# Performance work log

Hardware: AMD Instinct MI355X
Metric: run time of the kernel (lower is better)

The kernel has to match this reference:

```python
import jax, jax.numpy as jnp
import numpy as np

B, P = 4096, 32
NUM_ENTITY = 100000
NUM_METAPATH = 3
EMBED = 128
MAX_LEN = 3
C1, C2 = 128, 32


def setup_inputs() -> dict:
    key = jax.random.key(0)
    ks = jax.random.split(key, 20)
    inp = {}
    for g, L in enumerate([1, 2, 3]):
        inp[f"ent{L}"] = jax.random.randint(ks[3 * g], (B, P, L + 1), 0, NUM_ENTITY, dtype=jnp.int32)
        inp[f"mid{L}"] = jax.random.randint(ks[3 * g + 1], (B, P, L), 0, NUM_METAPATH, dtype=jnp.int32)
        inp[f"counts{L}"] = jax.random.uniform(ks[3 * g + 2], (B, P), jnp.float32, 0.5, 1.5)
    # parameters
    inp["E"] = jax.random.normal(ks[9], (NUM_ENTITY, EMBED), jnp.float32) * 0.02
    inp["W"] = jax.random.normal(ks[10], (NUM_METAPATH, EMBED), jnp.float32) * 0.1 + 1.0
    inp["Bm"] = jax.random.normal(ks[11], (NUM_METAPATH, EMBED), jnp.float32) * 0.02
    d_in = 2 * EMBED * MAX_LEN  # 768
    inp["W1"] = jax.random.normal(ks[12], (d_in, C1), jnp.float32) * (1.0 / np.sqrt(d_in))
    inp["b1"] = jnp.zeros((C1,), jnp.float32)
    inp["W2"] = jax.random.normal(ks[13], (C1, C2), jnp.float32) * (1.0 / np.sqrt(C1))
    inp["b2"] = jnp.zeros((C2,), jnp.float32)
    inp["W3"] = jax.random.normal(ks[14], (C2, 1), jnp.float32) * (1.0 / np.sqrt(C2))
    inp["b3"] = jnp.zeros((1,), jnp.float32)
    return inp


def _group_output(E, W, Bm, ents, mids, counts):
    """Vectorized forward_path over [B, P] paths of fixed length L, then
    count-weighted average over the P paths. ents: [B,P,L+1], mids: [B,P,L]."""
    L = mids.shape[-1]
    # forward direction
    x = E[ents[..., 0]]  # [B,P,EMBED]
    y = x
    for i in range(L):
        y = E[ents[..., i + 1]]
        x = jax.nn.relu(x * W[mids[..., i]] * y + Bm[mids[..., i]])
    out1 = x
    # backward direction: original code reuses stale y (embed of last entity)
    x = E[ents[..., L]]
    for i in reversed(range(L)):
        x = jax.nn.relu(x * W[mids[..., i]] * y + Bm[mids[..., i]])
    out2 = x
    path_out = jnp.concatenate([out1, out2], axis=-1)  # [B,P,2*EMBED]
    num = jnp.einsum("bp,bpe->be", counts, path_out)
    return num / jnp.sum(counts, axis=1, keepdims=True)  # [B,2*EMBED]


def reference(ent1, mid1, ent2, mid2, ent3, mid3, counts1, counts2, counts3,
              E, W, Bm, W1, b1, W2, b2, W3, b3):
    g1 = _group_output(E, W, Bm, ent1, mid1, counts1)
    g2 = _group_output(E, W, Bm, ent2, mid2, counts2)
    g3 = _group_output(E, W, Bm, ent3, mid3, counts3)
    h = jnp.concatenate([g1, g2, g3], axis=1)  # [B, 768]
    h = jax.nn.relu(h @ W1 + b1)
    h = jax.nn.relu(h @ W2 + b2)
    return h @ W3 + b3  # [B, 1]
```

## Files before the change

kernel.cpp:

```cpp
#include <hip/hip_runtime.h>

#define EMBED 128
#define NPATH 32
#define BATCH 4096
#define DIN 768
#define C1 128
#define C2 32

__device__ __forceinline__ float4 chain_step(float4 x, float4 y, float4 wm, float4 bm) {
    float4 r;
    r.x = fmaxf(fmaf(x.x * wm.x, y.x, bm.x), 0.f);
    r.y = fmaxf(fmaf(x.y * wm.y, y.y, bm.y), 0.f);
    r.z = fmaxf(fmaf(x.z * wm.z, y.z, bm.z), 0.f);
    r.w = fmaxf(fmaf(x.w * wm.w, y.w, bm.w), 0.f);
    return r;
}

template<int L>
__device__ __forceinline__ void group_body(
    int b, const int* __restrict__ ent, const int* __restrict__ mid,
    const float* __restrict__ counts, const float4* __restrict__ E4,
    const float4* __restrict__ W4, const float4* __restrict__ B4,
    float* __restrict__ h, int gcol, int* s_idx, float4* s_red, float4* s_wb)
{
    const int tid = threadIdx.x;
    const int dl = tid & 31;
    const int pq = tid >> 5;

    int* s_ent = s_idx;
    int* s_mid = s_idx + NPATH * (L + 1);
    float* s_cnt = (float*)(s_idx + NPATH * (2 * L + 1));
    float4* s_w4 = s_wb;
    float4* s_b4 = s_wb + 96;

    const int* entb = ent + (size_t)b * (NPATH * (L + 1));
    const int* midb = mid + (size_t)b * (NPATH * L);
    for (int i = tid; i < NPATH * (L + 1); i += 256) s_ent[i] = entb[i];
    for (int i = tid; i < NPATH * L; i += 256) s_mid[i] = midb[i];
    if (tid < NPATH) s_cnt[tid] = counts[(size_t)b * NPATH + tid];
    if (tid < 96) { s_w4[tid] = W4[tid]; s_b4[tid] = B4[tid]; }
    __syncthreads();

    float4 n1 = make_float4(0.f, 0.f, 0.f, 0.f);
    float4 n2 = make_float4(0.f, 0.f, 0.f, 0.f);

#pragma unroll 2
    for (int j = 0; j < NPATH / 8; ++j) {
        const int p = pq + 8 * j;
        int ei[L + 1], mi[L];
#pragma unroll
        for (int i = 0; i <= L; ++i) ei[i] = s_ent[p * (L + 1) + i];
#pragma unroll
        for (int i = 0; i < L; ++i) mi[i] = s_mid[p * L + i];

        float4 e[L + 1];
#pragma unroll
        for (int i = 0; i <= L; ++i) e[i] = E4[(size_t)ei[i] * 32 + dl];

        float4 wv[L], bv[L];
#pragma unroll
        for (int i = 0; i < L; ++i) {
            wv[i] = s_w4[mi[i] * 32 + dl];
            bv[i] = s_b4[mi[i] * 32 + dl];
        }
        const float c = s_cnt[p];

        float4 x = e[0];
#pragma unroll
        for (int i = 0; i < L; ++i)
            x = chain_step(x, e[i + 1], wv[i], bv[i]);

        const float4 yl = e[L];
        float4 x2 = yl;
#pragma unroll
        for (int i = L - 1; i >= 0; --i)
            x2 = chain_step(x2, yl, wv[i], bv[i]);

        n1.x = fmaf(c, x.x, n1.x); n1.y = fmaf(c, x.y, n1.y);
        n1.z = fmaf(c, x.z, n1.z); n1.w = fmaf(c, x.w, n1.w);
        n2.x = fmaf(c, x2.x, n2.x); n2.y = fmaf(c, x2.y, n2.y);
        n2.z = fmaf(c, x2.z, n2.z); n2.w = fmaf(c, x2.w, n2.w);
    }

    s_red[(pq * 2 + 0) * 32 + dl] = n1;
    s_red[(pq * 2 + 1) * 32 + dl] = n2;
    __syncthreads();
    if (tid < 64) {
        const int half = tid >> 5, dq = tid & 31;
        float4 a = s_red[(0 * 2 + half) * 32 + dq];
#pragma unroll
        for (int q = 1; q < 8; ++q) {
            float4 t = s_red[(q * 2 + half) * 32 + dq];
            a.x += t.x; a.y += t.y; a.z += t.z; a.w += t.w;
        }
        float den = 0.f;
#pragma unroll
        for (int p = 0; p < NPATH; ++p) den += s_cnt[p];
        const float inv = 1.f / den;
        a.x *= inv; a.y *= inv; a.z *= inv; a.w *= inv;
        float4* hb = (float4*)(h + (size_t)b * DIN + gcol);
        hb[half * 32 + dq] = a;
    }
}

__global__ __launch_bounds__(256) void groups_kernel(
    const int* __restrict__ e1, const int* __restrict__ m1, const float* __restrict__ c1,
    const int* __restrict__ e2, const int* __restrict__ m2, const float* __restrict__ c2,
    const int* __restrict__ e3, const int* __restrict__ m3, const float* __restrict__ c3,
    const float* __restrict__ E, const float* __restrict__ W, const float* __restrict__ Bm,
    float* __restrict__ h)
{
    __shared__ int s_idx[NPATH * 7 + NPATH];
    __shared__ float4 s_red[8 * 2 * 32];
    __shared__ float4 s_wb[192];
    const float4* E4 = (const float4*)E;
    const float4* W4 = (const float4*)W;
    const float4* B4 = (const float4*)Bm;
    const int bx = blockIdx.x;
    const int g = bx % 3;
    const int b = bx / 3;
    if (g == 0)      group_body<1>(b, e1, m1, c1, E4, W4, B4, h, 0,   s_idx, s_red, s_wb);
    else if (g == 1) group_body<2>(b, e2, m2, c2, E4, W4, B4, h, 256, s_idx, s_red, s_wb);
    else             group_body<3>(b, e3, m3, c3, E4, W4, B4, h, 512, s_idx, s_red, s_wb);
}

#define MROWS 8
#define KC 96
__global__ __launch_bounds__(256) void mlp_kernel(
    const float* __restrict__ h,
    const float* __restrict__ W1, const float* __restrict__ b1,
    const float* __restrict__ W2, const float* __restrict__ b2,
    const float* __restrict__ W3, const float* __restrict__ b3,
    float* __restrict__ out)
{
    __shared__ float hs[MROWS * DIN];
    __shared__ float w1s[KC * C1];
    __shared__ float h1[MROWS][C1];
    __shared__ float h2[MROWS][C2];

    const int tid = threadIdx.x;
    const int c = tid & 127;
    const int rh = tid >> 7;
    const int row0 = blockIdx.x * MROWS;

    {
        const float4* src = (const float4*)(h + (size_t)row0 * DIN);
        float4* dst = (float4*)hs;
#pragma unroll
        for (int i = 0; i < (MROWS * DIN / 4) / 256; ++i)
            dst[tid + i * 256] = src[tid + i * 256];
    }

    float acc[4];
    const float bias1 = b1[c];
#pragma unroll
    for (int r = 0; r < 4; ++r) acc[r] = bias1;

    const float* hrow = hs + rh * 4 * DIN;
    for (int ch = 0; ch < DIN / KC; ++ch) {
        {
            const float4* wsrc = (const float4*)(W1 + (size_t)ch * KC * C1);
            float4* wdst = (float4*)w1s;
#pragma unroll
            for (int i = 0; i < (KC * C1 / 4) / 256; ++i)
                wdst[tid + i * 256] = wsrc[tid + i * 256];
        }
        __syncthreads();

        const int kb = ch * KC;
#pragma unroll 4
        for (int k0 = 0; k0 < KC; k0 += 4) {
            const float w0 = w1s[(k0 + 0) * C1 + c];
            const float w1v = w1s[(k0 + 1) * C1 + c];
            const float w2v = w1s[(k0 + 2) * C1 + c];
            const float w3v = w1s[(k0 + 3) * C1 + c];
#pragma unroll
            for (int r = 0; r < 4; ++r) {
                const float4 hq = *(const float4*)(hrow + r * DIN + kb + k0);
                acc[r] = fmaf(hq.x, w0, acc[r]);
                acc[r] = fmaf(hq.y, w1v, acc[r]);
                acc[r] = fmaf(hq.z, w2v, acc[r]);
                acc[r] = fmaf(hq.w, w3v, acc[r]);
            }
        }
        __syncthreads();
    }

#pragma unroll
    for (int r = 0; r < 4; ++r) h1[rh * 4 + r][c] = fmaxf(acc[r], 0.f);
    __syncthreads();

    {
        const int r = tid >> 5;
        const int c2 = tid & 31;
        float a = b2[c2];
#pragma unroll
        for (int k = 0; k < C1; ++k)
            a = fmaf(h1[r][k], W2[k * C2 + c2], a);
        h2[r][c2] = fmaxf(a, 0.f);
    }
    __syncthreads();

    if (tid < MROWS) {
        float a = b3[0];
#pragma unroll
        for (int k = 0; k < C2; ++k)
            a = fmaf(h2[tid][k], W3[k], a);
        out[row0 + tid] = a;
    }
}

extern "C" void kernel_launch(void* const* d_in, const int* in_sizes, int n_in,
                              void* d_out, int out_size, void* d_ws, size_t ws_size,
                              hipStream_t stream) {
    const int*   ent1 = (const int*)d_in[0];
    const int*   mid1 = (const int*)d_in[1];
    const float* cnt1 = (const float*)d_in[2];
    const int*   ent2 = (const int*)d_in[3];
    const int*   mid2 = (const int*)d_in[4];
    const float* cnt2 = (const float*)d_in[5];
    const int*   ent3 = (const int*)d_in[6];
    const int*   mid3 = (const int*)d_in[7];
    const float* cnt3 = (const float*)d_in[8];
    const float* E    = (const float*)d_in[9];
    const float* W    = (const float*)d_in[10];
    const float* Bm   = (const float*)d_in[11];
    const float* W1   = (const float*)d_in[12];
    const float* b1   = (const float*)d_in[13];
    const float* W2   = (const float*)d_in[14];
    const float* b2   = (const float*)d_in[15];
    const float* W3   = (const float*)d_in[16];
    const float* b3   = (const float*)d_in[17];

    float* h = (float*)d_ws;
    float* out = (float*)d_out;

    groups_kernel<<<3 * BATCH, 256, 0, stream>>>(ent1, mid1, cnt1, ent2, mid2, cnt2,
                                                 ent3, mid3, cnt3, E, W, Bm, h);
    mlp_kernel<<<BATCH / MROWS, 256, 0, stream>>>(h, W1, b1, W2, b2, W3, b3, out);
}
```

Measured before the change: 223.3 us.

## Restructure MLP kernel to 1024 threads, 16 rows, direct global W1 reads

The first MLP layer now runs with 1024-thread blocks covering 16 rows, each thread computing two rows for one output column. W1 is read straight from global memory (through cache) rather than staged in LDS chunks, which removes the per-chunk barriers and shared-memory weight tile. The price is more global/L2 traffic for W1 per block and fewer rows per thread, so there is less register-level reuse of each weight load.

```diff
diff --git a/kernel.cpp b/kernel.cpp
--- a/kernel.cpp
+++ b/kernel.cpp
@@ -124,9 +124,8 @@
     else             group_body<3>(b, e3, m3, c3, E4, W4, B4, h, 512, s_idx, s_red, s_wb);
 }
 
-#define MROWS 8
-#define KC 96
-__global__ __launch_bounds__(256) void mlp_kernel(
+#define MROWS 16
+__global__ __launch_bounds__(1024) void mlp_kernel(
     const float* __restrict__ h,
     const float* __restrict__ W1, const float* __restrict__ b1,
     const float* __restrict__ W2, const float* __restrict__ b2,
@@ -134,63 +133,67 @@
     float* __restrict__ out)
 {
     __shared__ float hs[MROWS * DIN];
-    __shared__ float w1s[KC * C1];
     __shared__ float h1[MROWS][C1];
     __shared__ float h2[MROWS][C2];
 
     const int tid = threadIdx.x;
     const int c = tid & 127;
-    const int rh = tid >> 7;
+    const int rp = tid >> 7;
     const int row0 = blockIdx.x * MROWS;
 
     {
         const float4* src = (const float4*)(h + (size_t)row0 * DIN);
         float4* dst = (float4*)hs;
 #pragma unroll
-        for (int i = 0; i < (MROWS * DIN / 4) / 256; ++i)
-            dst[tid + i * 256] = src[tid + i * 256];
-    }
-
-    float acc[4];
-    const float bias1 = b1[c];
-#pragma unroll
-    for (int r = 0; r < 4; ++r) acc[r] = bias1;
-
-    const float* hrow = hs + rh * 4 * DIN;
-    for (int ch = 0; ch < DIN / KC; ++ch) {
-        {
-            const float4* wsrc = (const float4*)(W1 + (size_t)ch * KC * C1);
-            float4* wdst = (float4*)w1s;
-#pragma unroll
-            for (int i = 0; i < (KC * C1 / 4) / 256; ++i)
-                wdst[tid + i * 256] = wsrc[tid + i * 256];
-        }
-        __syncthreads();
-
-        const int kb = ch * KC;
-#pragma unroll 4
-        for (int k0 = 0; k0 < KC; k0 += 4) {
-            const float w0 = w1s[(k0 + 0) * C1 + c];
-            const float w1v = w1s[(k0 + 1) * C1 + c];
-            const float w2v = w1s[(k0 + 2) * C1 + c];
-            const float w3v = w1s[(k0 + 3) * C1 + c];
-#pragma unroll
-            for (int r = 0; r < 4; ++r) {
-                const float4 hq = *(const float4*)(hrow + r * DIN + kb + k0);
-                acc[r] = fmaf(hq.x, w0, acc[r]);
-                acc[r] = fmaf(hq.y, w1v, acc[r]);
-                acc[r] = fmaf(hq.z, w2v, acc[r]);
-                acc[r] = fmaf(hq.w, w3v, acc[r]);
-            }
-        }
-        __syncthreads();
-    }
-
-#pragma unroll
-    for (int r = 0; r < 4; ++r) h1[rh * 4 + r][c] = fmaxf(acc[r], 0.f);
-    __syncthreads();
-
-    {
+        for (int i = 0; i < 3; ++i)
+            dst[tid + i * 1024] = src[tid + i * 1024];
+    }
+    __syncthreads();
+
+    float acc0 = b1[c];
+    float acc1 = b1[c];
+    const float* h0 = hs + (2 * rp + 0) * DIN;
+    const float* h1p = hs + (2 * rp + 1) * DIN;
+
+    for (int k0 = 0; k0 < DIN; k0 += 8) {
+        float w0 = W1[(k0 + 0) * C1 + c];
+        float w1 = W1[(k0 + 1) * C1 + c];
+        float w2 = W1[(k0 + 2) * C1 + c];
+        float w3 = W1[(k0 + 3) * C1 + c];
+        float w4 = W1[(k0 + 4) * C1 + c];
+        float w5 = W1[(k0 + 5) * C1 + c];
+        float w6 = W1[(k0 + 6) * C1 + c];
+        float w7 = W1[(k0 + 7) * C1 + c];
+
+        const float4 a0 = *(const float4*)(h0 + k0);
+        const float4 a1 = *(const float4*)(h0 + k0 + 4);
+        const float4 b0 = *(const float4*)(h1p + k0);
+        const float4 b1q = *(const float4*)(h1p + k0 + 4);
+
+        acc0 = fmaf(a0.x, w0, acc0);
+        acc0 = fmaf(a0.y, w1, acc0);
+        acc0 = fmaf(a0.z, w2, acc0);
+        acc0 = fmaf(a0.w, w3, acc0);
+        acc0 = fmaf(a1.x, w4, acc0);
+        acc0 = fmaf(a1.y, w5, acc0);
+        acc0 = fmaf(a1.z, w6, acc0);
+        acc0 = fmaf(a1.w, w7, acc0);
+
+        acc1 = fmaf(b0.x, w0, acc1);
+        acc1 = fmaf(b0.y, w1, acc1);
+        acc1 = fmaf(b0.z, w2, acc1);
+        acc1 = fmaf(b0.w, w3, acc1);
+        acc1 = fmaf(b1q.x, w4, acc1);
+        acc1 = fmaf(b1q.y, w5, acc1);
+        acc1 = fmaf(b1q.z, w6, acc1);
+        acc1 = fmaf(b1q.w, w7, acc1);
+    }
+
+    h1[2 * rp + 0][c] = fmaxf(acc0, 0.f);
+    h1[2 * rp + 1][c] = fmaxf(acc1, 0.f);
+    __syncthreads();
+
+    if (tid < MROWS * C2) {
         const int r = tid >> 5;
         const int c2 = tid & 31;
         float a = b2[c2];
@@ -237,5 +240,5 @@
 
     groups_kernel<<<3 * BATCH, 256, 0, stream>>>(ent1, mid1, cnt1, ent2, mid2, cnt2,
                                                  ent3, mid3, cnt3, E, W, Bm, h);
-    mlp_kernel<<<BATCH / MROWS, 256, 0, stream>>>(h, W1, b1, W2, b2, W3, b3, out);
-}
+    mlp_kernel<<<BATCH / MROWS, 1024, 0, stream>>>(h, W1, b1, W2, b2, W3, b3, out);
+}
```

Measured after the change: 218.3 us. 2.2% less time.

## Double-buffer W1 chunks in MLP kernel with register prefetch

Applied to the files above, without the earlier changes.

Shrinks the W1 shared-memory chunk from 96 to 32 rows and double-buffers it. The next chunk is loaded from global memory into registers while the current chunk is computed, then stored to the alternate buffer. This removes one barrier per chunk and hides W1 load latency, at the cost of more chunk iterations and extra registers. The MLP kernel is likely a small part of total time next to the gather-heavy groups kernel.

```diff
diff --git a/kernel.cpp b/kernel.cpp
--- a/kernel.cpp
+++ b/kernel.cpp
@@ -125,7 +125,7 @@
 }
 
 #define MROWS 8
-#define KC 96
+#define KC 32
 __global__ __launch_bounds__(256) void mlp_kernel(
     const float* __restrict__ h,
     const float* __restrict__ W1, const float* __restrict__ b1,
@@ -134,7 +134,7 @@
     float* __restrict__ out)
 {
     __shared__ float hs[MROWS * DIN];
-    __shared__ float w1s[KC * C1];
+    __shared__ float w1s[2][KC * C1];
     __shared__ float h1[MROWS][C1];
     __shared__ float h2[MROWS][C2];
 
@@ -151,29 +151,39 @@
             dst[tid + i * 256] = src[tid + i * 256];
     }
 
+    {
+        const float4* wsrc = (const float4*)W1;
+        float4* wdst = (float4*)w1s[0];
+#pragma unroll
+        for (int i = 0; i < 4; ++i)
+            wdst[tid + i * 256] = wsrc[tid + i * 256];
+    }
+    __syncthreads();
+
     float acc[4];
     const float bias1 = b1[c];
 #pragma unroll
     for (int r = 0; r < 4; ++r) acc[r] = bias1;
 
     const float* hrow = hs + rh * 4 * DIN;
-    for (int ch = 0; ch < DIN / KC; ++ch) {
-        {
-            const float4* wsrc = (const float4*)(W1 + (size_t)ch * KC * C1);
-            float4* wdst = (float4*)w1s;
-#pragma unroll
-            for (int i = 0; i < (KC * C1 / 4) / 256; ++i)
-                wdst[tid + i * 256] = wsrc[tid + i * 256];
-        }
-        __syncthreads();
-
+    const int NCH = DIN / KC;
+    for (int ch = 0; ch < NCH; ++ch) {
+        float4 wreg[4];
+        if (ch + 1 < NCH) {
+            const float4* wsrc = (const float4*)(W1 + (size_t)(ch + 1) * KC * C1);
+#pragma unroll
+            for (int i = 0; i < 4; ++i)
+                wreg[i] = wsrc[tid + i * 256];
+        }
+
+        const float* wbuf = w1s[ch & 1];
         const int kb = ch * KC;
 #pragma unroll 4
         for (int k0 = 0; k0 < KC; k0 += 4) {
-            const float w0 = w1s[(k0 + 0) * C1 + c];
-            const float w1v = w1s[(k0 + 1) * C1 + c];
-            const float w2v = w1s[(k0 + 2) * C1 + c];
-            const float w3v = w1s[(k0 + 3) * C1 + c];
+            const float w0 = wbuf[(k0 + 0) * C1 + c];
+            const float w1v = wbuf[(k0 + 1) * C1 + c];
+            const float w2v = wbuf[(k0 + 2) * C1 + c];
+            const float w3v = wbuf[(k0 + 3) * C1 + c];
 #pragma unroll
             for (int r = 0; r < 4; ++r) {
                 const float4 hq = *(const float4*)(hrow + r * DIN + kb + k0);
@@ -182,6 +192,13 @@
                 acc[r] = fmaf(hq.z, w2v, acc[r]);
                 acc[r] = fmaf(hq.w, w3v, acc[r]);
             }
+        }
+
+        if (ch + 1 < NCH) {
+            float4* wdst = (float4*)w1s[(ch + 1) & 1];
+#pragma unroll
+            for (int i = 0; i < 4; ++i)
+                wdst[tid + i * 256] = wreg[i];
         }
         __syncthreads();
     }
```

Measured after the change: 260.6 us. 16.7% more time.
